# Kernel optimization log

Hardware: AMD Instinct MI355X
Metric: run time of the kernel (lower is better)

Reference implementation:

```python
import jax, jax.numpy as jnp
import numpy as np

K = 7          # involution kernel size
P = 3          # padding = (K-1)//2
GC = 16        # group_channels in involution
EPS = 1e-5


def bn(x, g, b):
    # training-mode BatchNorm2d forward: per-channel batch stats over (B,H,W)
    m = jnp.mean(x, axis=(0, 2, 3), keepdims=True)
    v = jnp.var(x, axis=(0, 2, 3), keepdims=True)
    return (x - m) * jax.lax.rsqrt(v + EPS) * g[None, :, None, None] + b[None, :, None, None]


def conv1x1(x, w):
    # x: [B,C,H,W], w: [O,C] -> [B,O,H,W]
    return jnp.einsum('bchw,oc->bohw', x, w)


def unfold7(x):
    # torch F.unfold(kernel=7, pad=3, stride=1) -> [B, C, K*K, H, W] (C slowest, matching torch layout)
    B, C, H, W = x.shape
    xp = jnp.pad(x, ((0, 0), (0, 0), (P, P), (P, P)))
    return jnp.stack([xp[:, :, i:i + H, j:j + W] for i in range(K) for j in range(K)], axis=2)


def involution(x, wr, gr, br, ws):
    # kernel generation: 1x1 reduce -> BN -> ReLU -> 1x1 span to G*K*K per-pixel kernels
    B, C, H, W = x.shape
    G = C // GC
    t = jax.nn.relu(bn(conv1x1(x, wr), gr, br))          # [B, C//4, H, W]
    w = conv1x1(t, ws).reshape(B, G, 1, K * K, H, W)     # per-pixel kernels
    p = unfold7(x).reshape(B, G, GC, K * K, H, W)        # unfolded patches
    return jnp.sum(w * p, axis=3).reshape(B, C, H, W)    # multiply-accumulate over K*K


def setup_inputs() -> dict:
    key = jax.random.key(0)
    ks = jax.random.split(key, 14)
    Cin, Cout, mid = 256, 256, 64
    red = mid // 4                 # reduction_ratio = 4
    G = mid // GC                  # groups = 4
    s = lambda *sh: 1.0 / np.sqrt(np.prod(sh[1:]) if len(sh) > 1 else sh[0])
    return {
        'x':  jax.random.normal(ks[0], (8, Cin, 56, 56), jnp.float32),
        'w1': jax.random.normal(ks[1], (mid, Cin), jnp.float32) * s(mid, Cin),
        'g1': jnp.ones((mid,), jnp.float32),
        'b1': jnp.zeros((mid,), jnp.float32),
        'wr': jax.random.normal(ks[2], (red, mid), jnp.float32) * s(red, mid),
        'gr': jnp.ones((red,), jnp.float32),
        'br': jnp.zeros((red,), jnp.float32),
        'ws': jax.random.normal(ks[3], (K * K * G, red), jnp.float32) * s(K * K * G, red),
        'g2': jnp.ones((mid,), jnp.float32),
        'b2': jnp.zeros((mid,), jnp.float32),
        'w3': jax.random.normal(ks[4], (Cout, mid), jnp.float32) * s(Cout, mid),
        'g3': jnp.ones((Cout,), jnp.float32),
        'b3': jnp.zeros((Cout,), jnp.float32),
    }


def reference(x, w1, g1, b1, wr, gr, br, ws, g2, b2, w3, g3, b3):
    out = jax.nn.relu(bn(conv1x1(x, w1), g1, b1))        # conv1 1x1 + BN + ReLU
    out = jax.nn.relu(bn(involution(out, wr, gr, br, ws), g2, b2))  # involution + BN + ReLU
    out = bn(conv1x1(out, w3), g3, b3)                   # conv3 1x1 + BN
    return jax.nn.relu(out + x)                          # residual add + ReLU
```

## Files before the change

### kernel.cpp

```cpp
#include <hip/hip_runtime.h>

#define HW 3136
#define NPIX 25088
#define NBLK 392

#define OFF_Y1   0u
#define OFF_TR   1605632u
#define OFF_WT   2007040u
#define OFF_OUT2 6924288u
#define OFF_Y3   8529920u
#define OFF_ST   14952448u
#define ACC1 0
#define ACCR 128
#define ACC2 160
#define ACC3 288
#define FIN1 800
#define FINR 928
#define FIN2 960
#define FIN3 1088

__device__ __forceinline__ float wave_sum(float v) {
    #pragma unroll
    for (int off = 32; off > 0; off >>= 1) v += __shfl_xor(v, off, 64);
    return v;
}

__global__ __launch_bounds__(256) void k_wt(const float* __restrict__ w1,
        const float* __restrict__ w3, float* __restrict__ w1t, float* __restrict__ w3t) {
    int i = blockIdx.x * 256 + threadIdx.x;
    if (i < 16384) {
        int oc = i >> 8, ic = i & 255;
        w1t[ic * 64 + oc] = w1[i];
    } else {
        int j = i - 16384;
        int oc = j >> 6, ic = j & 63;
        w3t[ic * 256 + oc] = w3[j];
    }
}

__global__ __launch_bounds__(128, 4) void k_conv1(const float* __restrict__ x,
        const float* __restrict__ w1t, float* __restrict__ y1, float* __restrict__ st) {
    __shared__ float xs[64][32];
    __shared__ float ws[64][64];
    int t = threadIdx.x, pb = blockIdx.x;
    int b = pb / 98, hw0 = (pb % 98) * 32;
    int tx = t & 7, ty = t >> 3;
    const size_t xbase = (size_t)(b * 256) * HW + hw0;

    float4 px[4], pw[8];
    #pragma unroll
    for (int i = 0; i < 4; i++) {
        int e = i * 128 + t, ic = e >> 3, p4 = e & 7;
        px[i] = *(const float4*)&x[xbase + (size_t)ic * HW + p4 * 4];
    }
    #pragma unroll
    for (int i = 0; i < 8; i++) {
        int e = i * 128 + t, ic = e >> 4, q = e & 15;
        pw[i] = *(const float4*)&w1t[ic * 64 + q * 4];
    }

    float acc[4][4];
    #pragma unroll
    for (int i = 0; i < 4; i++)
        #pragma unroll
        for (int j = 0; j < 4; j++) acc[i][j] = 0.f;

    #pragma unroll 1
    for (int cc = 0; cc < 4; cc++) {
        #pragma unroll
        for (int i = 0; i < 4; i++) {
            int e = i * 128 + t, ic = e >> 3, p4 = e & 7;
            *(float4*)&xs[ic][p4 * 4] = px[i];
        }
        #pragma unroll
        for (int i = 0; i < 8; i++) {
            int e = i * 128 + t, ic = e >> 4, q = e & 15;
            *(float4*)&ws[ic][q * 4] = pw[i];
        }
        __syncthreads();
        if (cc < 3) {
            #pragma unroll
            for (int i = 0; i < 4; i++) {
                int e = i * 128 + t, ic = e >> 3, p4 = e & 7;
                px[i] = *(const float4*)&x[xbase + (size_t)((cc + 1) * 64 + ic) * HW + p4 * 4];
            }
            #pragma unroll
            for (int i = 0; i < 8; i++) {
                int e = i * 128 + t, ic = e >> 4, q = e & 15;
                pw[i] = *(const float4*)&w1t[((cc + 1) * 64 + ic) * 64 + q * 4];
            }
        }
        #pragma unroll 8
        for (int c = 0; c < 64; c++) {
            float4 xv = *(const float4*)&xs[c][tx * 4];
            float4 wv = *(const float4*)&ws[c][ty * 4];
            float xa[4] = {xv.x, xv.y, xv.z, xv.w};
            float wa[4] = {wv.x, wv.y, wv.z, wv.w};
            #pragma unroll
            for (int i = 0; i < 4; i++)
                #pragma unroll
                for (int j = 0; j < 4; j++) acc[i][j] = fmaf(wa[i], xa[j], acc[i][j]);
        }
        __syncthreads();
    }
    #pragma unroll
    for (int i = 0; i < 4; i++) {
        int oc = ty * 4 + i;
        float4 o = make_float4(acc[i][0], acc[i][1], acc[i][2], acc[i][3]);
        *(float4*)&y1[((b * 64) + oc) * HW + hw0 + tx * 4] = o;
        float s = o.x + o.y + o.z + o.w;
        float q = o.x * o.x + o.y * o.y + o.z * o.z + o.w * o.w;
        #pragma unroll
        for (int off = 1; off <= 4; off <<= 1) {
            s += __shfl_xor(s, off, 64);
            q += __shfl_xor(q, off, 64);
        }
        if (tx == 0) {
            atomicAdd(&st[ACC1 + oc], s);
            atomicAdd(&st[ACC1 + 64 + oc], q);
        }
    }
}

__global__ void k_fin(const float* __restrict__ acc, float* __restrict__ fin,
                      const float* __restrict__ gamma, const float* __restrict__ beta, int C) {
    int c = threadIdx.x;
    if (c < C) {
        float mean = acc[c] * (1.0f / (float)NPIX);
        float var  = acc[C + c] * (1.0f / (float)NPIX) - mean * mean;
        float rstd = rsqrtf(var + 1e-5f);
        float a = gamma[c] * rstd;
        fin[c] = a;
        fin[C + c] = beta[c] - mean * a;
    }
}

__global__ __launch_bounds__(256, 4) void k_bn1_convr(float* __restrict__ y1,
        const float* __restrict__ wr, float* __restrict__ tr, float* __restrict__ st) {
    __shared__ float ys[64][64];
    __shared__ float wsh[16][64];
    int t = threadIdx.x, pb = blockIdx.x;
    int b = pb / 49, hw0 = (pb % 49) * 64;
    int tx = t & 15, ty = t >> 4;
    #pragma unroll
    for (int i = 0; i < 16; i++) {
        int e = i * 256 + t, c = e >> 6, p = e & 63;
        int gi = ((b * 64) + c) * HW + hw0 + p;
        float v = y1[gi];
        v = fmaxf(st[FIN1 + c] * v + st[FIN1 + 64 + c], 0.f);
        ys[c][p] = v;
        y1[gi] = v;
    }
    #pragma unroll
    for (int i = 0; i < 4; i++) {
        int e = i * 256 + t;
        wsh[e >> 6][e & 63] = wr[e];
    }
    __syncthreads();
    float a0 = 0.f, a1 = 0.f, a2 = 0.f, a3 = 0.f;
    #pragma unroll 8
    for (int c = 0; c < 64; c++) {
        float4 yv = *(const float4*)&ys[c][tx * 4];
        float wv = wsh[ty][c];
        a0 = fmaf(wv, yv.x, a0); a1 = fmaf(wv, yv.y, a1);
        a2 = fmaf(wv, yv.z, a2); a3 = fmaf(wv, yv.w, a3);
    }
    *(float4*)&tr[((b * 16) + ty) * HW + hw0 + tx * 4] = make_float4(a0, a1, a2, a3);
    float s = a0 + a1 + a2 + a3;
    float q = a0 * a0 + a1 * a1 + a2 * a2 + a3 * a3;
    #pragma unroll
    for (int off = 1; off <= 8; off <<= 1) {
        s += __shfl_xor(s, off, 64);
        q += __shfl_xor(q, off, 64);
    }
    if (tx == 0) {
        atomicAdd(&st[ACCR + ty], s);
        atomicAdd(&st[ACCR + 16 + ty], q);
    }
}

__global__ __launch_bounds__(256) void k_invol(const float* __restrict__ y1r,
        const float* __restrict__ tr, const float* __restrict__ wsp,
        float* __restrict__ out2, float* __restrict__ st) {
    __shared__ float ts[16][256];
    __shared__ float sw[49][16];
    __shared__ float ps[8][10][64];
    __shared__ float red[4][16];
    int t = threadIdx.x, bidx = blockIdx.x;
    int h = bidx & 1, r2 = bidx >> 1;
    int ht = r2 % 14;
    int bg = r2 / 14;
    int g = bg & 3, b = bg >> 2;
    int h0 = ht * 4;
    int c0 = h * 8;
    #pragma unroll
    for (int i = 0; i < 16; i++) {
        int e = i * 256 + t, c = e >> 8, p = e & 255;
        if (p < 224) {
            float v = tr[((b * 16) + c) * HW + h0 * 56 + p];
            ts[c][p] = fmaxf(st[FINR + c] * v + st[FINR + 16 + c], 0.f);
        }
    }
    for (int e = t; e < 784; e += 256) sw[e >> 4][e & 15] = wsp[g * 784 + e];
    for (int i = 0; i < 20; i++) {
        int e = i * 256 + t;
        int c = e / 640, rem = e - c * 640;
        int r = rem >> 6, wc = rem & 63;
        int gh = h0 + r - 3, gw = wc - 3;
        float v = 0.f;
        if (gh >= 0 && gh < 56 && gw >= 0 && gw < 56)
            v = y1r[((b * 64) + g * 16 + c0 + c) * HW + gh * 56 + gw];
        ps[c][r][wc] = v;
    }
    __syncthreads();
    float accv[8];
    #pragma unroll
    for (int c = 0; c < 8; c++) accv[c] = 0.f;
    bool active = t < 224;
    if (active) {
        int lh = t / 56, lw = t % 56;
        float tsr[16];
        #pragma unroll
        for (int c = 0; c < 16; c++) tsr[c] = ts[c][t];
        float kr[49];
        #pragma unroll
        for (int k = 0; k < 49; k++) {
            const float4* swr = (const float4*)&sw[k][0];
            float4 u0 = swr[0], u1 = swr[1], u2 = swr[2], u3 = swr[3];
            float v = u0.x * tsr[0];
            v = fmaf(u0.y, tsr[1], v);  v = fmaf(u0.z, tsr[2], v);  v = fmaf(u0.w, tsr[3], v);
            v = fmaf(u1.x, tsr[4], v);  v = fmaf(u1.y, tsr[5], v);  v = fmaf(u1.z, tsr[6], v);
            v = fmaf(u1.w, tsr[7], v);  v = fmaf(u2.x, tsr[8], v);  v = fmaf(u2.y, tsr[9], v);
            v = fmaf(u2.z, tsr[10], v); v = fmaf(u2.w, tsr[11], v); v = fmaf(u3.x, tsr[12], v);
            v = fmaf(u3.y, tsr[13], v); v = fmaf(u3.z, tsr[14], v); v = fmaf(u3.w, tsr[15], v);
            kr[k] = v;
        }
        #pragma unroll
        for (int k = 0; k < 49; k++) {
            int ki = k / 7, kj = k % 7;
            float kv = kr[k];
            #pragma unroll
            for (int c = 0; c < 8; c++)
                accv[c] = fmaf(kv, ps[c][lh + ki][lw + kj], accv[c]);
        }
        int hw = h0 * 56 + t;
        #pragma unroll
        for (int c = 0; c < 8; c++)
            out2[((b * 64) + g * 16 + c0 + c) * HW + hw] = accv[c];
    }
    int wave = t >> 6, lane = t & 63;
    #pragma unroll
    for (int c = 0; c < 8; c++) {
        float v = active ? accv[c] : 0.f;
        float s  = wave_sum(v);
        float s2 = wave_sum(v * v);
        if (lane == 0) { red[wave][c] = s; red[wave][8 + c] = s2; }
    }
    __syncthreads();
    if (t < 16) {
        float s = red[0][t] + red[1][t] + red[2][t] + red[3][t];
        int c = t & 7, isq = t >> 3;
        atomicAdd(&st[ACC2 + isq * 64 + g * 16 + c0 + c], s);
    }
}

__global__ __launch_bounds__(256, 4) void k_bn2_conv3(const float* __restrict__ out2,
        const float* __restrict__ w3t, float* __restrict__ y3, float* __restrict__ st) {
    __shared__ float os[64][64];
    __shared__ float wst[64][64];
    int t = threadIdx.x, blk = blockIdx.x;
    int occ = blk & 3, pb = blk >> 2;
    int b = pb / 49, hw0 = (pb % 49) * 64;
    int tx = t & 15, ty = t >> 4;
    #pragma unroll
    for (int i = 0; i < 16; i++) {
        int e = i * 256 + t, c = e >> 6, p = e & 63;
        float v = out2[((b * 64) + c) * HW + hw0 + p];
        os[c][p] = fmaxf(st[FIN2 + c] * v + st[FIN2 + 64 + c], 0.f);
        wst[c][p] = w3t[c * 256 + occ * 64 + p];
    }
    __syncthreads();
    float acc[4][4];
    #pragma unroll
    for (int i = 0; i < 4; i++)
        #pragma unroll
        for (int j = 0; j < 4; j++) acc[i][j] = 0.f;
    #pragma unroll 8
    for (int c = 0; c < 64; c++) {
        float4 xv = *(const float4*)&os[c][tx * 4];
        float4 wv = *(const float4*)&wst[c][ty * 4];
        float xa[4] = {xv.x, xv.y, xv.z, xv.w};
        float wa[4] = {wv.x, wv.y, wv.z, wv.w};
        #pragma unroll
        for (int i = 0; i < 4; i++)
            #pragma unroll
            for (int j = 0; j < 4; j++) acc[i][j] = fmaf(wa[i], xa[j], acc[i][j]);
    }
    #pragma unroll
    for (int i = 0; i < 4; i++) {
        int oc = occ * 64 + ty * 4 + i;
        float4 o = make_float4(acc[i][0], acc[i][1], acc[i][2], acc[i][3]);
        *(float4*)&y3[((b * 256) + oc) * HW + hw0 + tx * 4] = o;
        float s = o.x + o.y + o.z + o.w;
        float q = o.x * o.x + o.y * o.y + o.z * o.z + o.w * o.w;
        #pragma unroll
        for (int off = 1; off <= 8; off <<= 1) {
            s += __shfl_xor(s, off, 64);
            q += __shfl_xor(q, off, 64);
        }
        if (tx == 0) {
            atomicAdd(&st[ACC3 + oc], s);
            atomicAdd(&st[ACC3 + 256 + oc], q);
        }
    }
}

__global__ __launch_bounds__(256) void k_final(const float* __restrict__ y3,
        const float* __restrict__ x, float* __restrict__ out, const float* __restrict__ st) {
    int idx = blockIdx.x * 256 + threadIdx.x;
    if (idx < 1605632) {
        int c = (idx / 784) & 255;
        float a = st[FIN3 + c], bb = st[FIN3 + 256 + c];
        float4 v  = ((const float4*)y3)[idx];
        float4 xv = ((const float4*)x)[idx];
        float4 o;
        o.x = fmaxf(a * v.x + bb + xv.x, 0.f);
        o.y = fmaxf(a * v.y + bb + xv.y, 0.f);
        o.z = fmaxf(a * v.z + bb + xv.z, 0.f);
        o.w = fmaxf(a * v.w + bb + xv.w, 0.f);
        ((float4*)out)[idx] = o;
    }
}

extern "C" void kernel_launch(void* const* d_in, const int* in_sizes, int n_in,
                              void* d_out, int out_size, void* d_ws, size_t ws_size,
                              hipStream_t stream) {
    const float* x   = (const float*)d_in[0];
    const float* w1  = (const float*)d_in[1];
    const float* g1  = (const float*)d_in[2];
    const float* b1  = (const float*)d_in[3];
    const float* wr  = (const float*)d_in[4];
    const float* gr  = (const float*)d_in[5];
    const float* br  = (const float*)d_in[6];
    const float* wsp = (const float*)d_in[7];
    const float* g2  = (const float*)d_in[8];
    const float* b2  = (const float*)d_in[9];
    const float* w3  = (const float*)d_in[10];
    const float* g3  = (const float*)d_in[11];
    const float* b3  = (const float*)d_in[12];
    float* out = (float*)d_out;
    float* w   = (float*)d_ws;
    float* y1   = w + OFF_Y1;
    float* tr   = w + OFF_TR;
    float* w1t  = w + OFF_WT;
    float* w3t  = w + OFF_WT + 16384;
    float* out2 = w + OFF_OUT2;
    float* y3   = w + OFF_Y3;
    float* st   = w + OFF_ST;

    hipMemsetAsync(st, 0, 2048 * sizeof(float), stream);
    k_wt<<<128, 256, 0, stream>>>(w1, w3, w1t, w3t);
    k_conv1<<<784, 128, 0, stream>>>(x, w1t, y1, st);
    k_fin<<<1, 64, 0, stream>>>(st + ACC1, st + FIN1, g1, b1, 64);
    k_bn1_convr<<<NBLK, 256, 0, stream>>>(y1, wr, tr, st);
    k_fin<<<1, 64, 0, stream>>>(st + ACCR, st + FINR, gr, br, 16);
    k_invol<<<896, 256, 0, stream>>>(y1, tr, wsp, out2, st);
    k_fin<<<1, 64, 0, stream>>>(st + ACC2, st + FIN2, g2, b2, 64);
    k_bn2_conv3<<<NBLK * 4, 256, 0, stream>>>(out2, w3t, y3, st);
    k_fin<<<1, 256, 0, stream>>>(st + ACC3, st + FIN3, g3, b3, 256);
    k_final<<<6272, 256, 0, stream>>>(y3, x, out, st);
}
```

Baseline: 332.0 us.

## Shrink per-block tiles across conv and involution kernels to launch more blocks

Halves or quarters the pixel and channel tiles handled by each block in conv1, bn1+convr, involution and bn2+conv3, and doubles or quadruples the grid sizes to match. conv1 drops its register-prefetch double buffering in favour of direct loads each channel chunk. The aim is more blocks in flight to fill the GPU's compute units and hide latency. The cost is lower arithmetic intensity per thread, narrower float2 and scalar memory accesses, more redundant halo and weight loads in the involution, and more atomics on the statistics buffer.

```diff
diff --git a/kernel.cpp b/kernel.cpp
--- a/kernel.cpp
+++ b/kernel.cpp
@@ -2,7 +2,6 @@
 
 #define HW 3136
 #define NPIX 25088
-#define NBLK 392
 
 #define OFF_Y1   0u
 #define OFF_TR   1605632u
@@ -40,76 +39,47 @@
 
 __global__ __launch_bounds__(128, 4) void k_conv1(const float* __restrict__ x,
         const float* __restrict__ w1t, float* __restrict__ y1, float* __restrict__ st) {
-    __shared__ float xs[64][32];
+    __shared__ float xs[64][16];
     __shared__ float ws[64][64];
     int t = threadIdx.x, pb = blockIdx.x;
-    int b = pb / 98, hw0 = (pb % 98) * 32;
+    int b = pb / 196, hw0 = (pb % 196) * 16;
     int tx = t & 7, ty = t >> 3;
-    const size_t xbase = (size_t)(b * 256) * HW + hw0;
-
-    float4 px[4], pw[8];
-    #pragma unroll
-    for (int i = 0; i < 4; i++) {
-        int e = i * 128 + t, ic = e >> 3, p4 = e & 7;
-        px[i] = *(const float4*)&x[xbase + (size_t)ic * HW + p4 * 4];
-    }
-    #pragma unroll
-    for (int i = 0; i < 8; i++) {
-        int e = i * 128 + t, ic = e >> 4, q = e & 15;
-        pw[i] = *(const float4*)&w1t[ic * 64 + q * 4];
-    }
-
-    float acc[4][4];
-    #pragma unroll
-    for (int i = 0; i < 4; i++)
-        #pragma unroll
-        for (int j = 0; j < 4; j++) acc[i][j] = 0.f;
-
+    float a0[4], a1[4];
+    #pragma unroll
+    for (int j = 0; j < 4; j++) { a0[j] = 0.f; a1[j] = 0.f; }
     #pragma unroll 1
     for (int cc = 0; cc < 4; cc++) {
         #pragma unroll
-        for (int i = 0; i < 4; i++) {
-            int e = i * 128 + t, ic = e >> 3, p4 = e & 7;
-            *(float4*)&xs[ic][p4 * 4] = px[i];
+        for (int i = 0; i < 8; i++) {
+            int e = i * 128 + t, c = e >> 4, p = e & 15;
+            xs[c][p] = x[((b * 256) + cc * 64 + c) * HW + hw0 + p];
         }
         #pragma unroll
         for (int i = 0; i < 8; i++) {
             int e = i * 128 + t, ic = e >> 4, q = e & 15;
-            *(float4*)&ws[ic][q * 4] = pw[i];
+            *(float4*)&ws[ic][q * 4] = *(const float4*)&w1t[(cc * 64 + ic) * 64 + q * 4];
         }
         __syncthreads();
-        if (cc < 3) {
-            #pragma unroll
-            for (int i = 0; i < 4; i++) {
-                int e = i * 128 + t, ic = e >> 3, p4 = e & 7;
-                px[i] = *(const float4*)&x[xbase + (size_t)((cc + 1) * 64 + ic) * HW + p4 * 4];
-            }
-            #pragma unroll
-            for (int i = 0; i < 8; i++) {
-                int e = i * 128 + t, ic = e >> 4, q = e & 15;
-                pw[i] = *(const float4*)&w1t[((cc + 1) * 64 + ic) * 64 + q * 4];
-            }
-        }
         #pragma unroll 8
         for (int c = 0; c < 64; c++) {
-            float4 xv = *(const float4*)&xs[c][tx * 4];
+            float2 xv = *(const float2*)&xs[c][tx * 2];
             float4 wv = *(const float4*)&ws[c][ty * 4];
-            float xa[4] = {xv.x, xv.y, xv.z, xv.w};
             float wa[4] = {wv.x, wv.y, wv.z, wv.w};
             #pragma unroll
-            for (int i = 0; i < 4; i++)
-                #pragma unroll
-                for (int j = 0; j < 4; j++) acc[i][j] = fmaf(wa[i], xa[j], acc[i][j]);
+            for (int j = 0; j < 4; j++) {
+                a0[j] = fmaf(wa[j], xv.x, a0[j]);
+                a1[j] = fmaf(wa[j], xv.y, a1[j]);
+            }
         }
         __syncthreads();
     }
     #pragma unroll
-    for (int i = 0; i < 4; i++) {
-        int oc = ty * 4 + i;
-        float4 o = make_float4(acc[i][0], acc[i][1], acc[i][2], acc[i][3]);
-        *(float4*)&y1[((b * 64) + oc) * HW + hw0 + tx * 4] = o;
-        float s = o.x + o.y + o.z + o.w;
-        float q = o.x * o.x + o.y * o.y + o.z * o.z + o.w * o.w;
+    for (int j = 0; j < 4; j++) {
+        int oc = ty * 4 + j;
+        float2 o = make_float2(a0[j], a1[j]);
+        *(float2*)&y1[((b * 64) + oc) * HW + hw0 + tx * 2] = o;
+        float s = o.x + o.y;
+        float q = o.x * o.x + o.y * o.y;
         #pragma unroll
         for (int off = 1; off <= 4; off <<= 1) {
             s += __shfl_xor(s, off, 64);
@@ -135,16 +105,16 @@
     }
 }
 
-__global__ __launch_bounds__(256, 4) void k_bn1_convr(float* __restrict__ y1,
+__global__ __launch_bounds__(128, 4) void k_bn1_convr(float* __restrict__ y1,
         const float* __restrict__ wr, float* __restrict__ tr, float* __restrict__ st) {
-    __shared__ float ys[64][64];
-    __shared__ float wsh[16][64];
+    __shared__ float ys[64][16];
+    __shared__ float wsh[16][68];
     int t = threadIdx.x, pb = blockIdx.x;
-    int b = pb / 49, hw0 = (pb % 49) * 64;
-    int tx = t & 15, ty = t >> 4;
-    #pragma unroll
-    for (int i = 0; i < 16; i++) {
-        int e = i * 256 + t, c = e >> 6, p = e & 63;
+    int b = pb / 196, hw0 = (pb % 196) * 16;
+    int tx = t & 7, ty = t >> 3;
+    #pragma unroll
+    for (int i = 0; i < 8; i++) {
+        int e = i * 128 + t, c = e >> 4, p = e & 15;
         int gi = ((b * 64) + c) * HW + hw0 + p;
         float v = y1[gi];
         v = fmaxf(st[FIN1 + c] * v + st[FIN1 + 64 + c], 0.f);
@@ -152,24 +122,24 @@
         y1[gi] = v;
     }
     #pragma unroll
-    for (int i = 0; i < 4; i++) {
-        int e = i * 256 + t;
+    for (int i = 0; i < 8; i++) {
+        int e = i * 128 + t;
         wsh[e >> 6][e & 63] = wr[e];
     }
     __syncthreads();
-    float a0 = 0.f, a1 = 0.f, a2 = 0.f, a3 = 0.f;
+    float a0 = 0.f, a1 = 0.f;
     #pragma unroll 8
     for (int c = 0; c < 64; c++) {
-        float4 yv = *(const float4*)&ys[c][tx * 4];
+        float2 yv = *(const float2*)&ys[c][tx * 2];
         float wv = wsh[ty][c];
-        a0 = fmaf(wv, yv.x, a0); a1 = fmaf(wv, yv.y, a1);
-        a2 = fmaf(wv, yv.z, a2); a3 = fmaf(wv, yv.w, a3);
-    }
-    *(float4*)&tr[((b * 16) + ty) * HW + hw0 + tx * 4] = make_float4(a0, a1, a2, a3);
-    float s = a0 + a1 + a2 + a3;
-    float q = a0 * a0 + a1 * a1 + a2 * a2 + a3 * a3;
-    #pragma unroll
-    for (int off = 1; off <= 8; off <<= 1) {
+        a0 = fmaf(wv, yv.x, a0);
+        a1 = fmaf(wv, yv.y, a1);
+    }
+    *(float2*)&tr[((b * 16) + ty) * HW + hw0 + tx * 2] = make_float2(a0, a1);
+    float s = a0 + a1;
+    float q = a0 * a0 + a1 * a1;
+    #pragma unroll
+    for (int off = 1; off <= 4; off <<= 1) {
         s += __shfl_xor(s, off, 64);
         q += __shfl_xor(q, off, 64);
     }
@@ -184,15 +154,15 @@
         float* __restrict__ out2, float* __restrict__ st) {
     __shared__ float ts[16][256];
     __shared__ float sw[49][16];
-    __shared__ float ps[8][10][64];
-    __shared__ float red[4][16];
+    __shared__ float ps[4][10][64];
+    __shared__ float red[4][8];
     int t = threadIdx.x, bidx = blockIdx.x;
-    int h = bidx & 1, r2 = bidx >> 1;
+    int h = bidx & 3, r2 = bidx >> 2;
     int ht = r2 % 14;
     int bg = r2 / 14;
     int g = bg & 3, b = bg >> 2;
     int h0 = ht * 4;
-    int c0 = h * 8;
+    int c0 = h * 4;
     #pragma unroll
     for (int i = 0; i < 16; i++) {
         int e = i * 256 + t, c = e >> 8, p = e & 255;
@@ -202,7 +172,8 @@
         }
     }
     for (int e = t; e < 784; e += 256) sw[e >> 4][e & 15] = wsp[g * 784 + e];
-    for (int i = 0; i < 20; i++) {
+    #pragma unroll
+    for (int i = 0; i < 10; i++) {
         int e = i * 256 + t;
         int c = e / 640, rem = e - c * 640;
         int r = rem >> 6, wc = rem & 63;
@@ -213,9 +184,9 @@
         ps[c][r][wc] = v;
     }
     __syncthreads();
-    float accv[8];
-    #pragma unroll
-    for (int c = 0; c < 8; c++) accv[c] = 0.f;
+    float accv[4];
+    #pragma unroll
+    for (int c = 0; c < 4; c++) accv[c] = 0.f;
     bool active = t < 224;
     if (active) {
         int lh = t / 56, lw = t % 56;
@@ -240,71 +211,73 @@
             int ki = k / 7, kj = k % 7;
             float kv = kr[k];
             #pragma unroll
-            for (int c = 0; c < 8; c++)
+            for (int c = 0; c < 4; c++)
                 accv[c] = fmaf(kv, ps[c][lh + ki][lw + kj], accv[c]);
         }
         int hw = h0 * 56 + t;
         #pragma unroll
-        for (int c = 0; c < 8; c++)
+        for (int c = 0; c < 4; c++)
             out2[((b * 64) + g * 16 + c0 + c) * HW + hw] = accv[c];
     }
     int wave = t >> 6, lane = t & 63;
     #pragma unroll
-    for (int c = 0; c < 8; c++) {
+    for (int c = 0; c < 4; c++) {
         float v = active ? accv[c] : 0.f;
         float s  = wave_sum(v);
         float s2 = wave_sum(v * v);
-        if (lane == 0) { red[wave][c] = s; red[wave][8 + c] = s2; }
+        if (lane == 0) { red[wave][c] = s; red[wave][4 + c] = s2; }
     }
     __syncthreads();
-    if (t < 16) {
+    if (t < 8) {
         float s = red[0][t] + red[1][t] + red[2][t] + red[3][t];
-        int c = t & 7, isq = t >> 3;
+        int c = t & 3, isq = t >> 2;
         atomicAdd(&st[ACC2 + isq * 64 + g * 16 + c0 + c], s);
     }
 }
 
-__global__ __launch_bounds__(256, 4) void k_bn2_conv3(const float* __restrict__ out2,
+__global__ __launch_bounds__(128, 4) void k_bn2_conv3(const float* __restrict__ out2,
         const float* __restrict__ w3t, float* __restrict__ y3, float* __restrict__ st) {
-    __shared__ float os[64][64];
-    __shared__ float wst[64][64];
+    __shared__ float xs[64][16];
+    __shared__ float ws[64][64];
     int t = threadIdx.x, blk = blockIdx.x;
-    int occ = blk & 3, pb = blk >> 2;
-    int b = pb / 49, hw0 = (pb % 49) * 64;
-    int tx = t & 15, ty = t >> 4;
-    #pragma unroll
-    for (int i = 0; i < 16; i++) {
-        int e = i * 256 + t, c = e >> 6, p = e & 63;
+    int os = blk & 3, pb = blk >> 2;
+    int b = pb / 196, hw0 = (pb % 196) * 16;
+    int tx = t & 7, ty = t >> 3;
+    #pragma unroll
+    for (int i = 0; i < 8; i++) {
+        int e = i * 128 + t, c = e >> 4, p = e & 15;
         float v = out2[((b * 64) + c) * HW + hw0 + p];
-        os[c][p] = fmaxf(st[FIN2 + c] * v + st[FIN2 + 64 + c], 0.f);
-        wst[c][p] = w3t[c * 256 + occ * 64 + p];
+        xs[c][p] = fmaxf(st[FIN2 + c] * v + st[FIN2 + 64 + c], 0.f);
+    }
+    #pragma unroll
+    for (int i = 0; i < 8; i++) {
+        int e = i * 128 + t, ic = e >> 4, q = e & 15;
+        *(float4*)&ws[ic][q * 4] = *(const float4*)&w3t[ic * 256 + os * 64 + q * 4];
     }
     __syncthreads();
-    float acc[4][4];
-    #pragma unroll
-    for (int i = 0; i < 4; i++)
-        #pragma unroll
-        for (int j = 0; j < 4; j++) acc[i][j] = 0.f;
+    float a0[4], a1[4];
+    #pragma unroll
+    for (int j = 0; j < 4; j++) { a0[j] = 0.f; a1[j] = 0.f; }
     #pragma unroll 8
     for (int c = 0; c < 64; c++) {
-        float4 xv = *(const float4*)&os[c][tx * 4];
-        float4 wv = *(const float4*)&wst[c][ty * 4];
-        float xa[4] = {xv.x, xv.y, xv.z, xv.w};
+        float2 xv = *(const float2*)&xs[c][tx * 2];
+        float4 wv = *(const float4*)&ws[c][ty * 4];
         float wa[4] = {wv.x, wv.y, wv.z, wv.w};
         #pragma unroll
-        for (int i = 0; i < 4; i++)
-            #pragma unroll
-            for (int j = 0; j < 4; j++) acc[i][j] = fmaf(wa[i], xa[j], acc[i][j]);
-    }
-    #pragma unroll
-    for (int i = 0; i < 4; i++) {
-        int oc = occ * 64 + ty * 4 + i;
-        float4 o = make_float4(acc[i][0], acc[i][1], acc[i][2], acc[i][3]);
-        *(float4*)&y3[((b * 256) + oc) * HW + hw0 + tx * 4] = o;
-        float s = o.x + o.y + o.z + o.w;
-        float q = o.x * o.x + o.y * o.y + o.z * o.z + o.w * o.w;
-        #pragma unroll
-        for (int off = 1; off <= 8; off <<= 1) {
+        for (int j = 0; j < 4; j++) {
+            a0[j] = fmaf(wa[j], xv.x, a0[j]);
+            a1[j] = fmaf(wa[j], xv.y, a1[j]);
+        }
+    }
+    #pragma unroll
+    for (int j = 0; j < 4; j++) {
+        int oc = os * 64 + ty * 4 + j;
+        float2 o = make_float2(a0[j], a1[j]);
+        *(float2*)&y3[((b * 256) + oc) * HW + hw0 + tx * 2] = o;
+        float s = o.x + o.y;
+        float q = o.x * o.x + o.y * o.y;
+        #pragma unroll
+        for (int off = 1; off <= 4; off <<= 1) {
             s += __shfl_xor(s, off, 64);
             q += __shfl_xor(q, off, 64);
         }
@@ -360,13 +333,13 @@
 
     hipMemsetAsync(st, 0, 2048 * sizeof(float), stream);
     k_wt<<<128, 256, 0, stream>>>(w1, w3, w1t, w3t);
-    k_conv1<<<784, 128, 0, stream>>>(x, w1t, y1, st);
+    k_conv1<<<1568, 128, 0, stream>>>(x, w1t, y1, st);
     k_fin<<<1, 64, 0, stream>>>(st + ACC1, st + FIN1, g1, b1, 64);
-    k_bn1_convr<<<NBLK, 256, 0, stream>>>(y1, wr, tr, st);
+    k_bn1_convr<<<1568, 128, 0, stream>>>(y1, wr, tr, st);
     k_fin<<<1, 64, 0, stream>>>(st + ACCR, st + FINR, gr, br, 16);
-    k_invol<<<896, 256, 0, stream>>>(y1, tr, wsp, out2, st);
+    k_invol<<<1792, 256, 0, stream>>>(y1, tr, wsp, out2, st);
     k_fin<<<1, 64, 0, stream>>>(st + ACC2, st + FIN2, g2, b2, 64);
-    k_bn2_conv3<<<NBLK * 4, 256, 0, stream>>>(out2, w3t, y3, st);
+    k_bn2_conv3<<<6272, 128, 0, stream>>>(out2, w3t, y3, st);
     k_fin<<<1, 256, 0, stream>>>(st + ACC3, st + FIN3, g3, b3, 256);
     k_final<<<6272, 256, 0, stream>>>(y3, x, out, st);
 }
```

Result: slower. 523.8 us (+57.8%).
